# Kernel tuning notes

Hardware: AMD Instinct MI355X
Metric: run time of the kernel (lower is better)

## Reference

```python
import jax, jax.numpy as jnp
import numpy as np

IN_F, OUT_F, BLOCK, NBLK = 1024, 4096, 256, 16
TOPK = NBLK // 4  # 4, as in forward: n_blocks // 4


def setup_inputs() -> dict:
    key = jax.random.key(0)
    ks = jax.random.split(key, 7)
    s = 1.0 / np.sqrt(IN_F)
    s2 = 1.0 / np.sqrt(OUT_F)
    return {
        "x": jax.random.normal(ks[0], (4, 4096, IN_F), jnp.float32),
        "router_w": jax.random.uniform(ks[1], (NBLK, IN_F), jnp.float32, -s, s),
        "router_b": jax.random.uniform(ks[2], (NBLK,), jnp.float32, -s, s),
        "w1": jax.random.uniform(ks[3], (OUT_F, IN_F), jnp.float32, -s, s),
        "b1": jax.random.uniform(ks[4], (OUT_F,), jnp.float32, -s, s),
        "w2": jax.random.uniform(ks[5], (IN_F, OUT_F), jnp.float32, -s2, s2),
        "b2": jax.random.uniform(ks[6], (IN_F,), jnp.float32, -s2, s2),
    }


def reference(x, router_w, router_b, w1, b1, w2, b2):
    x_shape = x.shape
    xf = x.reshape(-1, IN_F)  # [N, d]
    n = xf.shape[0]
    # router: Linear + softmax, then top-k block selection per token
    prob = jax.nn.softmax(xf @ router_w.T + router_b, axis=-1)  # [N, n_blocks]
    _, idx = jax.lax.top_k(prob, TOPK)  # [N, k]
    mask = jnp.zeros((n, NBLK), bool).at[jnp.arange(n)[:, None], idx].set(True)
    # RoutedLinearRow: per-block fc1, zeros at unselected blocks
    w1b = w1.reshape(NBLK, BLOCK, IN_F)
    b1b = b1.reshape(NBLK, BLOCK)
    h = jnp.einsum('nd,ibd->nib', xf, w1b) + b1b  # [N, n_blocks, block]
    h = jnp.where(mask[:, :, None], h, jnp.zeros((), h.dtype))
    h = jax.nn.relu(h)
    # RoutedLinearCol: only selected blocks contribute
    w2b = w2.reshape(IN_F, NBLK, BLOCK)
    y = jnp.einsum('nib,dib->nd', jnp.where(mask[:, :, None], h, 0.0), w2b) + b2
    return y.reshape(x_shape)
```

## Files before the change

### kernel.cpp

```cpp
#include <hip/hip_runtime.h>
#include <hip/hip_bf16.h>

#define NTOK   16384
#define INF    1024
#define OUTF   4096
#define NBLK   16
#define BLKSZ  256
#define KTOP   4

typedef short bf16x8 __attribute__((ext_vector_type(8)));
typedef float f32x4 __attribute__((ext_vector_type(4)));
typedef unsigned short u16x8 __attribute__((ext_vector_type(8)));

__device__ __forceinline__ unsigned short f2bf(float f) {
  unsigned u = __float_as_uint(f);
  u += 0x7FFFu + ((u >> 16) & 1u);
  return (unsigned short)(u >> 16);
}

__device__ __forceinline__ void load_lds16(const void* g, void* l) {
  __builtin_amdgcn_global_load_lds(
      (const __attribute__((address_space(1))) unsigned int*)g,
      (__attribute__((address_space(3))) unsigned int*)l, 16, 0, 0);
}

__device__ __forceinline__ double shfl_xor_d(double v, int m) {
  long long l = __double_as_longlong(v);
  int lo = (int)(l & 0xFFFFFFFFll), hi = (int)(l >> 32);
  lo = __shfl_xor(lo, m);
  hi = __shfl_xor(hi, m);
  return __longlong_as_double(((long long)hi << 32) | (unsigned long long)(unsigned)lo);
}

__device__ __forceinline__ int pi_perm(int j) {
  return (j & 128) | ((j & 7) << 4) | ((j >> 3) & 15);
}

__global__ __launch_bounds__(256) void k_cvt_router(
    const float* __restrict__ x, const float* __restrict__ rw,
    const float* __restrict__ rb, const float* __restrict__ w1,
    const float* __restrict__ w2, const float* __restrict__ b1,
    unsigned* __restrict__ tok_blocks, unsigned* __restrict__ counts,
    unsigned short* __restrict__ xb, unsigned short* __restrict__ w1b,
    unsigned short* __restrict__ w2p, float* __restrict__ b1p) {
  __shared__ float4 rwl[4096];
  const int tid = threadIdx.x;
  const float4* rw4 = (const float4*)rw;
  for (int i = tid; i < 4096; i += 256) rwl[i] = rw4[i];
  __syncthreads();

  const int n = blockIdx.x * 32 + (tid >> 3);
  const int q = tid & 7;
  double p[16];
#pragma unroll
  for (int j = 0; j < 16; ++j) p[j] = 0.0;
  const float4* xr = (const float4*)(x + (size_t)n * INF);
  ushort4* xbr = (ushort4*)(xb + (size_t)n * INF);
#pragma unroll 4
  for (int i = 0; i < 32; ++i) {
    const int d4 = q + i * 8;
    const float4 xv = xr[d4];
    ushort4 o;
    o.x = f2bf(xv.x); o.y = f2bf(xv.y); o.z = f2bf(xv.z); o.w = f2bf(xv.w);
    xbr[d4] = o;
#pragma unroll
    for (int j = 0; j < 16; ++j) {
      const float4 wv = rwl[j * 256 + d4];
      p[j] = fma((double)xv.x, (double)wv.x, p[j]);
      p[j] = fma((double)xv.y, (double)wv.y, p[j]);
      p[j] = fma((double)xv.z, (double)wv.z, p[j]);
      p[j] = fma((double)xv.w, (double)wv.w, p[j]);
    }
  }
#pragma unroll
  for (int j = 0; j < 16; ++j) {
    double v = p[j];
    v += shfl_xor_d(v, 1);
    v += shfl_xor_d(v, 2);
    v += shfl_xor_d(v, 4);
    p[j] = v + (double)rb[j];
  }

  __syncthreads();
  unsigned* hist = (unsigned*)rwl;
  if (tid < 16) hist[tid] = 0;
  __syncthreads();

  if (q == 0) {
    unsigned packed = 0;
#pragma unroll
    for (int j = 0; j < 16; ++j) {
      int r = 0;
#pragma unroll
      for (int j2 = 0; j2 < 16; ++j2)
        r += (int)((p[j2] > p[j]) | ((p[j2] == p[j]) & (j2 < j)));
      if (r < KTOP) packed |= (unsigned)j << (8 * r);
    }
    tok_blocks[n] = packed;
    atomicAdd(&hist[packed & 15u], 1u);
    atomicAdd(&hist[(packed >> 8) & 15u], 1u);
    atomicAdd(&hist[(packed >> 16) & 15u], 1u);
    atomicAdd(&hist[(packed >> 24) & 15u], 1u);
  }
  __syncthreads();
  if (tid < 16 && hist[tid]) atomicAdd(&counts[tid], hist[tid]);

  const size_t stride = (size_t)gridDim.x * 256;
  for (size_t i = (size_t)blockIdx.x * 256 + tid; i < 1573376; i += stride) {
    if (i < 1048576) {
      float4 v = ((const float4*)w1)[i];
      ushort4 o;
      o.x = f2bf(v.x); o.y = f2bf(v.y); o.z = f2bf(v.z); o.w = f2bf(v.w);
      ((ushort4*)w1b)[i] = o;
    } else if (i < 1572864) {
      const size_t g = i - 1048576;
      const int d = (int)(g >> 9);
      const int rest = (int)(g & 511);
      const int jg = rest * 8;
      const int blk = jg >> 8;
      const int j0 = jg & 255;
      const float* src = w2 + (size_t)d * 4096 + blk * 256;
      u16x8 o;
#pragma unroll
      for (int ni = 0; ni < 8; ++ni) o[ni] = f2bf(src[pi_perm(j0 + ni)]);
      *(u16x8*)(w2p + (size_t)d * 4096 + jg) = o;
    } else {
      const int idx = (int)(i - 1572864);
      const int jg = idx * 8;
      const int blk = jg >> 8;
      const int j0 = jg & 255;
      const float* src = b1 + blk * 256;
      float o[8];
#pragma unroll
      for (int ni = 0; ni < 8; ++ni) o[ni] = src[pi_perm(j0 + ni)];
      float4* dst = (float4*)(b1p + jg);
      dst[0] = make_float4(o[0], o[1], o[2], o[3]);
      dst[1] = make_float4(o[4], o[5], o[6], o[7]);
    }
  }
}

__global__ __launch_bounds__(256) void k_build(
    const unsigned* __restrict__ tok_blocks, const unsigned* __restrict__ counts,
    unsigned* __restrict__ alloc, unsigned short* __restrict__ list) {
  unsigned offl[16];
  {
    unsigned o = 0;
#pragma unroll
    for (int i = 0; i < 16; ++i) { offl[i] = o; o += (counts[i] + 127u) & ~127u; }
  }
  const int n = blockIdx.x * 256 + threadIdx.x;
  const unsigned packed = tok_blocks[n];
  const int lane = threadIdx.x & 63;
#pragma unroll
  for (int b = 0; b < 16; ++b) {
    int r = -1;
#pragma unroll
    for (int q = 0; q < 4; ++q)
      if (((packed >> (8 * q)) & 15u) == (unsigned)b) r = q;
    unsigned long long m = __ballot(r >= 0);
    if (m) {
      int leader = __ffsll((unsigned long long)m) - 1;
      unsigned base = 0;
      if (lane == leader) base = offl[b] + atomicAdd(&alloc[b], (unsigned)__popcll(m));
      base = (unsigned)__shfl((int)base, leader);
      if (r >= 0) {
        unsigned pos = base + (unsigned)__popcll(m & ((1ull << lane) - 1ull));
        list[pos] = (unsigned short)(n | (r << 14));
      }
    }
  }
}

__global__ __launch_bounds__(256, 1) void k_ffn(
    const unsigned short* __restrict__ xb, const unsigned short* __restrict__ w1b,
    const unsigned short* __restrict__ w2p, const float* __restrict__ b1p,
    const unsigned short* __restrict__ list, const unsigned* __restrict__ counts,
    unsigned short* __restrict__ part) {
  __shared__ __align__(16) char lds[163840];
  char* const As0 = lds + 65536;
  char* const As1 = lds + 81920;
  char* const Bs0 = lds + 98304;
  char* const Bs1 = lds + 131072;

  const int bid0 = blockIdx.x;
  const int bid = (bid0 & 7) * 256 + (bid0 >> 3);
  const int blk = bid >> 7;
  const int tile = bid & 127;
  unsigned cnt = 0, goffBase = 0;
  {
    unsigned o = 0;
#pragma unroll
    for (int i = 0; i < 16; ++i) {
      const unsigned c = counts[i];
      if (i == blk) { cnt = c; goffBase = o; }
      o += (c + 127u) & ~127u;
    }
  }
  if ((unsigned)(tile * 128) >= cnt) return;
  const unsigned goff = goffBase + tile * 128;
  const int rem = (int)cnt - tile * 128;

  const int tid = threadIdx.x;
  const int lane = tid & 63;
  const int wid = tid >> 6;
  const int wr = wid >> 1;
  const int wc = wid & 1;
  const int c16 = lane & 15;
  const int aChunk = (tid & 7) ^ ((tid >> 3) & 7);

  unsigned tok[4];
#pragma unroll
  for (int l = 0; l < 4; ++l) tok[l] = list[goff + (tid >> 3) + l * 32] & 0x3FFFu;

#define STAGE_A(buf, k0)                                                        \
  _Pragma("unroll")                                                             \
  for (int l = 0; l < 4; ++l)                                                   \
    load_lds16(xb + (size_t)tok[l] * 1024 + (k0) + aChunk * 8,                  \
               (buf) + (l * 256 + wid * 64) * 16);

#define STAGE_B1(buf, k0)                                                       \
  _Pragma("unroll")                                                             \
  for (int l = 0; l < 8; ++l)                                                   \
    load_lds16(w1b + (size_t)(blk * 256 + l * 32 + (tid >> 3)) * 1024 + (k0) +  \
                   aChunk * 8,                                                  \
               (buf) + (l * 256 + wid * 64) * 16);

#define COMPUTE_A(abuf, bbuf)                                                   \
  _Pragma("unroll")                                                             \
  for (int ks = 0; ks < 2; ++ks) {                                              \
    const int kc = ks * 4 + (lane >> 4);                                        \
    bf16x8 a[4], b[8];                                                          \
    _Pragma("unroll")                                                           \
    for (int mi = 0; mi < 4; ++mi) {                                            \
      const int row = wr * 64 + mi * 16 + c16;                                  \
      a[mi] = *(const bf16x8*)((abuf) + row * 128 + ((kc ^ (row & 7)) << 4));   \
    }                                                                           \
    _Pragma("unroll")                                                           \
    for (int ni = 0; ni < 8; ++ni) {                                            \
      const int row = wc * 128 + ni * 16 + c16;                                 \
      b[ni] = *(const bf16x8*)((bbuf) + row * 128 + ((kc ^ (row & 7)) << 4));   \
    }                                                                           \
    _Pragma("unroll")                                                           \
    for (int mi = 0; mi < 4; ++mi)                                              \
      _Pragma("unroll")                                                         \
      for (int ni = 0; ni < 8; ++ni)                                            \
        acc[mi][ni] =                                                           \
            __builtin_amdgcn_mfma_f32_16x16x32_bf16(a[mi], b[ni], acc[mi][ni], 0, 0, 0); \
  }

  f32x4 acc[4][8] = {};
  STAGE_A(As0, 0);
  STAGE_B1(Bs0, 0);
  __syncthreads();
#pragma unroll 1
  for (int kk = 0; kk < 8; ++kk) {
    const int k0 = kk * 128;
    STAGE_A(As1, k0 + 64);
    STAGE_B1(Bs1, k0 + 64);
    COMPUTE_A(As0, Bs0);
    __syncthreads();
    if (kk < 7) {
      STAGE_A(As0, k0 + 128);
      STAGE_B1(Bs0, k0 + 128);
    }
    COMPUTE_A(As1, Bs1);
    __syncthreads();
  }

#define STAGE_B2(buf, it)                                                       \
  {                                                                             \
    const int ns2 = (it) >> 2, k02 = ((it) & 3) * 64;                           \
    _Pragma("unroll")                                                           \
    for (int l = 0; l < 8; ++l)                                                 \
      load_lds16(w2p + (size_t)(ns2 * 256 + l * 32 + (tid >> 3)) * 4096 +       \
                     blk * 256 + k02 + aChunk * 8,                              \
                 (buf) + (l * 256 + wid * 64) * 16);                            \
  }

#define COMPUTE_B(bbuf, k02)                                                    \
  _Pragma("unroll")                                                             \
  for (int ks = 0; ks < 2; ++ks) {                                              \
    const int kc = ks * 4 + (lane >> 4);                                        \
    bf16x8 a[4], b[8];                                                          \
    _Pragma("unroll")                                                           \
    for (int mi = 0; mi < 4; ++mi) {                                            \
      const int row = wr * 64 + mi * 16 + c16;                                  \
      a[mi] = *(const bf16x8*)(lds + row * 512 + (k02) * 2 +                    \
                               ((kc ^ (row & 7)) << 4));                        \
    }                                                                           \
    _Pragma("unroll")                                                           \
    for (int ni = 0; ni < 8; ++ni) {                                            \
      const int row = wc * 128 + ni * 16 + c16;                                 \
      b[ni] = *(const bf16x8*)((bbuf) + row * 128 + ((kc ^ (row & 7)) << 4));   \
    }                                                                           \
    _Pragma("unroll")                                                           \
    for (int mi = 0; mi < 4; ++mi)                                              \
      _Pragma("unroll")                                                         \
      for (int ni = 0; ni < 8; ++ni)                                            \
        acc2[mi][ni] =                                                          \
            __builtin_amdgcn_mfma_f32_16x16x32_bf16(a[mi], b[ni], acc2[mi][ni], 0, 0, 0); \
  }

  STAGE_B2(Bs0, 0);

  {
    const float4* bp = (const float4*)(b1p + blk * 256 + wc * 128 + c16 * 8);
    const float4 bv0 = bp[0], bv1 = bp[1];
    const float bvv[8] = {bv0.x, bv0.y, bv0.z, bv0.w, bv1.x, bv1.y, bv1.z, bv1.w};
    const int chunk = wc * 16 + c16;
    const int cslot = (chunk & ~7);
    const int clow  = (chunk & 7);
#pragma unroll
    for (int mi = 0; mi < 4; ++mi) {
#pragma unroll
      for (int i = 0; i < 4; ++i) {
        const int row = wr * 64 + mi * 16 + (lane >> 4) * 4 + i;
        u16x8 wv;
#pragma unroll
        for (int ni = 0; ni < 8; ++ni) {
          float v = acc[mi][ni][i] + bvv[ni];
          v = v > 0.f ? v : 0.f;
          wv[ni] = f2bf(v);
        }
        *(u16x8*)(lds + row * 512 + ((cslot | (clow ^ (row & 7))) << 4)) = wv;
      }
    }
  }
  __syncthreads();

#pragma unroll 1
  for (int ns = 0; ns < 4; ++ns) {
    f32x4 acc2[4][8] = {};
    const int it0 = ns * 4;
    STAGE_B2(Bs1, it0 + 1);
    COMPUTE_B(Bs0, 0);
    __syncthreads();
    STAGE_B2(Bs0, it0 + 2);
    COMPUTE_B(Bs1, 64);
    __syncthreads();
    STAGE_B2(Bs1, it0 + 3);
    COMPUTE_B(Bs0, 128);
    __syncthreads();
    if (ns < 3) STAGE_B2(Bs0, it0 + 4);
    COMPUTE_B(Bs1, 192);
    __syncthreads();
#pragma unroll
    for (int mi = 0; mi < 4; ++mi) {
#pragma unroll
      for (int i = 0; i < 4; ++i) {
        const int row = wr * 64 + mi * 16 + (lane >> 4) * 4 + i;
        if (row < rem) {
          const unsigned e = list[goff + row];
          u16x8 wv;
#pragma unroll
          for (int ni = 0; ni < 8; ++ni) wv[ni] = f2bf(acc2[mi][ni][i]);
          *(u16x8*)(part + ((size_t)(e & 0x3FFFu) * 4 + (e >> 14)) * 1024 +
                    ns * 256 + wc * 128 + c16 * 8) = wv;
        }
      }
    }
  }
#undef STAGE_A
#undef STAGE_B1
#undef STAGE_B2
#undef COMPUTE_A
#undef COMPUTE_B
}

__global__ __launch_bounds__(256) void k_reduce(const unsigned short* __restrict__ part,
                                                const float* __restrict__ b2,
                                                float* __restrict__ out) {
  __shared__ float lds[8 * 1028];
  const int tid = threadIdx.x;
  const int tok0 = blockIdx.x * 8;
  const int tok_l = tid >> 5;
  const int l32 = tid & 31;
  const unsigned short* pbase = part + (size_t)(tok0 + tok_l) * 4096;

#pragma unroll
  for (int g = 0; g < 4; ++g) {
    const int idx = g * 32 + l32;
    const int p0 = idx * 8;
    float s[8] = {0.f, 0.f, 0.f, 0.f, 0.f, 0.f, 0.f, 0.f};
#pragma unroll
    for (int sl = 0; sl < 4; ++sl) {
      u16x8 v = *(const u16x8*)(pbase + sl * 1024 + p0);
#pragma unroll
      for (int j = 0; j < 8; ++j)
        s[j] += __uint_as_float((unsigned)(unsigned short)v[j] << 16);
    }
    const int ns = idx >> 5, wcb = (idx >> 4) & 1, cc = idx & 15;
#pragma unroll
    for (int ni = 0; ni < 8; ++ni)
      lds[tok_l * 1028 + ns * 256 + wcb * 128 + ni * 16 + cc] = s[ni];
  }
  __syncthreads();
  const float4 b2v = ((const float4*)b2)[tid];
#pragma unroll
  for (int r = 0; r < 8; ++r) {
    f32x4 lv = *(f32x4*)&lds[r * 1028 + tid * 4];
    float4 o = make_float4(lv[0] + b2v.x, lv[1] + b2v.y, lv[2] + b2v.z, lv[3] + b2v.w);
    *(float4*)(out + (size_t)(tok0 + r) * 1024 + tid * 4) = o;
  }
}

extern "C" void kernel_launch(void* const* d_in, const int* in_sizes, int n_in,
                              void* d_out, int out_size, void* d_ws, size_t ws_size,
                              hipStream_t stream) {
  const float* x  = (const float*)d_in[0];
  const float* rw = (const float*)d_in[1];
  const float* rb = (const float*)d_in[2];
  const float* w1 = (const float*)d_in[3];
  const float* b1 = (const float*)d_in[4];
  const float* w2 = (const float*)d_in[5];
  const float* b2 = (const float*)d_in[6];
  float* out = (float*)d_out;

  char* ws = (char*)d_ws;
  unsigned short* part = (unsigned short*)(ws);
  unsigned short* xb   = (unsigned short*)(ws + 134217728);
  unsigned short* w1b  = (unsigned short*)(ws + 167772160);
  unsigned short* w2p  = (unsigned short*)(ws + 176160768);
  unsigned* tokb       = (unsigned*)(ws + 184549376);
  unsigned short* list = (unsigned short*)(ws + 184614912);
  float* b1p           = (float*)(ws + 184750080);
  unsigned* counts     = (unsigned*)(ws + 184766464);
  unsigned* alloc      = (unsigned*)(ws + 184766528);

  hipMemsetAsync(ws + 184766464, 0, 128, stream);
  k_cvt_router<<<dim3(512), dim3(256), 0, stream>>>(x, rw, rb, w1, w2, b1, tokb,
                                                    counts, xb, w1b, w2p, b1p);
  k_build<<<dim3(64), dim3(256), 0, stream>>>(tokb, counts, alloc, list);
  k_ffn<<<dim3(2048), dim3(256), 0, stream>>>(xb, w1b, w2p, b1p, list, counts, part);
  k_reduce<<<dim3(2048), dim3(256), 0, stream>>>(part, b2, out);
}
```

Before: 290.6 us.

## Split FFN workgroup across 8 waves with 64x64 per-wave tiles

```diff
diff --git a/kernel.cpp b/kernel.cpp
--- a/kernel.cpp
+++ b/kernel.cpp
@@ -11,6 +11,7 @@
 typedef short bf16x8 __attribute__((ext_vector_type(8)));
 typedef float f32x4 __attribute__((ext_vector_type(4)));
 typedef unsigned short u16x8 __attribute__((ext_vector_type(8)));
+typedef unsigned short u16x4 __attribute__((ext_vector_type(4)));
 
 __device__ __forceinline__ unsigned short f2bf(float f) {
   unsigned u = __float_as_uint(f);
@@ -32,8 +33,8 @@
   return __longlong_as_double(((long long)hi << 32) | (unsigned long long)(unsigned)lo);
 }
 
-__device__ __forceinline__ int pi_perm(int j) {
-  return (j & 128) | ((j & 7) << 4) | ((j >> 3) & 15);
+__device__ __forceinline__ int pi2(int j) {
+  return (j & 192) | ((j & 3) << 4) | ((j >> 2) & 15);
 }
 
 __global__ __launch_bounds__(256) void k_cvt_router(
@@ -122,7 +123,7 @@
       const float* src = w2 + (size_t)d * 4096 + blk * 256;
       u16x8 o;
 #pragma unroll
-      for (int ni = 0; ni < 8; ++ni) o[ni] = f2bf(src[pi_perm(j0 + ni)]);
+      for (int ni = 0; ni < 8; ++ni) o[ni] = f2bf(src[pi2(j0 + ni)]);
       *(u16x8*)(w2p + (size_t)d * 4096 + jg) = o;
     } else {
       const int idx = (int)(i - 1572864);
@@ -132,7 +133,7 @@
       const float* src = b1 + blk * 256;
       float o[8];
 #pragma unroll
-      for (int ni = 0; ni < 8; ++ni) o[ni] = src[pi_perm(j0 + ni)];
+      for (int ni = 0; ni < 8; ++ni) o[ni] = src[pi2(j0 + ni)];
       float4* dst = (float4*)(b1p + jg);
       dst[0] = make_float4(o[0], o[1], o[2], o[3]);
       dst[1] = make_float4(o[4], o[5], o[6], o[7]);
@@ -172,7 +173,7 @@
   }
 }
 
-__global__ __launch_bounds__(256, 1) void k_ffn(
+__global__ __launch_bounds__(512, 1) void k_ffn(
     const unsigned short* __restrict__ xb, const unsigned short* __restrict__ w1b,
     const unsigned short* __restrict__ w2p, const float* __restrict__ b1p,
     const unsigned short* __restrict__ list, const unsigned* __restrict__ counts,
@@ -204,52 +205,57 @@
   const int tid = threadIdx.x;
   const int lane = tid & 63;
   const int wid = tid >> 6;
-  const int wr = wid >> 1;
-  const int wc = wid & 1;
+  const int wr = wid >> 2;
+  const int wc = wid & 3;
+  const int asl = tid & 7;
   const int c16 = lane & 15;
-  const int aChunk = (tid & 7) ^ ((tid >> 3) & 7);
-
-  unsigned tok[4];
-#pragma unroll
-  for (int l = 0; l < 4; ++l) tok[l] = list[goff + (tid >> 3) + l * 32] & 0x3FFFu;
+
+  const unsigned tok0 = list[goff + (tid >> 3)] & 0x3FFFu;
+  const unsigned tok1 = list[goff + 64 + (tid >> 3)] & 0x3FFFu;
+  const int arow0 = tid >> 3;
+  const int arow1 = 64 + arow0;
 
 #define STAGE_A(buf, k0)                                                        \
-  _Pragma("unroll")                                                             \
-  for (int l = 0; l < 4; ++l)                                                   \
-    load_lds16(xb + (size_t)tok[l] * 1024 + (k0) + aChunk * 8,                  \
-               (buf) + (l * 256 + wid * 64) * 16);
+  {                                                                             \
+    load_lds16(xb + (size_t)tok0 * INF + (k0) + (asl ^ (arow0 & 7)) * 8,        \
+               (buf) + (wid * 64) * 16);                                        \
+    load_lds16(xb + (size_t)tok1 * INF + (k0) + (asl ^ (arow1 & 7)) * 8,        \
+               (buf) + (512 + wid * 64) * 16);                                  \
+  }
 
 #define STAGE_B1(buf, k0)                                                       \
   _Pragma("unroll")                                                             \
-  for (int l = 0; l < 8; ++l)                                                   \
-    load_lds16(w1b + (size_t)(blk * 256 + l * 32 + (tid >> 3)) * 1024 + (k0) +  \
-                   aChunk * 8,                                                  \
-               (buf) + (l * 256 + wid * 64) * 16);
+  for (int r = 0; r < 4; ++r) {                                                 \
+    const int row = (r * 512 + tid) >> 3;                                       \
+    load_lds16(w1b + ((size_t)(blk * 256 + row)) * INF + (k0) +                 \
+                   (asl ^ (row & 7)) * 8,                                       \
+               (buf) + (r * 512 + wid * 64) * 16);                              \
+  }
 
 #define COMPUTE_A(abuf, bbuf)                                                   \
   _Pragma("unroll")                                                             \
   for (int ks = 0; ks < 2; ++ks) {                                              \
     const int kc = ks * 4 + (lane >> 4);                                        \
-    bf16x8 a[4], b[8];                                                          \
+    bf16x8 a[4], b[4];                                                          \
     _Pragma("unroll")                                                           \
     for (int mi = 0; mi < 4; ++mi) {                                            \
       const int row = wr * 64 + mi * 16 + c16;                                  \
       a[mi] = *(const bf16x8*)((abuf) + row * 128 + ((kc ^ (row & 7)) << 4));   \
     }                                                                           \
     _Pragma("unroll")                                                           \
-    for (int ni = 0; ni < 8; ++ni) {                                            \
-      const int row = wc * 128 + ni * 16 + c16;                                 \
+    for (int ni = 0; ni < 4; ++ni) {                                            \
+      const int row = wc * 64 + ni * 16 + c16;                                  \
       b[ni] = *(const bf16x8*)((bbuf) + row * 128 + ((kc ^ (row & 7)) << 4));   \
     }                                                                           \
     _Pragma("unroll")                                                           \
     for (int mi = 0; mi < 4; ++mi)                                              \
       _Pragma("unroll")                                                         \
-      for (int ni = 0; ni < 8; ++ni)                                            \
+      for (int ni = 0; ni < 4; ++ni)                                            \
         acc[mi][ni] =                                                           \
             __builtin_amdgcn_mfma_f32_16x16x32_bf16(a[mi], b[ni], acc[mi][ni], 0, 0, 0); \
   }
 
-  f32x4 acc[4][8] = {};
+  f32x4 acc[4][4] = {};
   STAGE_A(As0, 0);
   STAGE_B1(Bs0, 0);
   __syncthreads();
@@ -272,17 +278,19 @@
   {                                                                             \
     const int ns2 = (it) >> 2, k02 = ((it) & 3) * 64;                           \
     _Pragma("unroll")                                                           \
-    for (int l = 0; l < 8; ++l)                                                 \
-      load_lds16(w2p + (size_t)(ns2 * 256 + l * 32 + (tid >> 3)) * 4096 +       \
-                     blk * 256 + k02 + aChunk * 8,                              \
-                 (buf) + (l * 256 + wid * 64) * 16);                            \
+    for (int r = 0; r < 4; ++r) {                                               \
+      const int row = (r * 512 + tid) >> 3;                                     \
+      load_lds16(w2p + (size_t)(ns2 * 256 + row) * OUTF + blk * 256 + k02 +     \
+                     (asl ^ (row & 7)) * 8,                                     \
+                 (buf) + (r * 512 + wid * 64) * 16);                            \
+    }                                                                           \
   }
 
 #define COMPUTE_B(bbuf, k02)                                                    \
   _Pragma("unroll")                                                             \
   for (int ks = 0; ks < 2; ++ks) {                                              \
     const int kc = ks * 4 + (lane >> 4);                                        \
-    bf16x8 a[4], b[8];                                                          \
+    bf16x8 a[4], b[4];                                                          \
     _Pragma("unroll")                                                           \
     for (int mi = 0; mi < 4; ++mi) {                                            \
       const int row = wr * 64 + mi * 16 + c16;                                  \
@@ -290,14 +298,14 @@
                                ((kc ^ (row & 7)) << 4));                        \
     }                                                                           \
     _Pragma("unroll")                                                           \
-    for (int ni = 0; ni < 8; ++ni) {                                            \
-      const int row = wc * 128 + ni * 16 + c16;                                 \
+    for (int ni = 0; ni < 4; ++ni) {                                            \
+      const int row = wc * 64 + ni * 16 + c16;                                  \
       b[ni] = *(const bf16x8*)((bbuf) + row * 128 + ((kc ^ (row & 7)) << 4));   \
     }                                                                           \
     _Pragma("unroll")                                                           \
     for (int mi = 0; mi < 4; ++mi)                                              \
       _Pragma("unroll")                                                         \
-      for (int ni = 0; ni < 8; ++ni)                                            \
+      for (int ni = 0; ni < 4; ++ni)                                            \
         acc2[mi][ni] =                                                          \
             __builtin_amdgcn_mfma_f32_16x16x32_bf16(a[mi], b[ni], acc2[mi][ni], 0, 0, 0); \
   }
@@ -305,25 +313,22 @@
   STAGE_B2(Bs0, 0);
 
   {
-    const float4* bp = (const float4*)(b1p + blk * 256 + wc * 128 + c16 * 8);
-    const float4 bv0 = bp[0], bv1 = bp[1];
-    const float bvv[8] = {bv0.x, bv0.y, bv0.z, bv0.w, bv1.x, bv1.y, bv1.z, bv1.w};
-    const int chunk = wc * 16 + c16;
-    const int cslot = (chunk & ~7);
-    const int clow  = (chunk & 7);
+    const float4 bv = *(const float4*)(b1p + blk * 256 + wc * 64 + c16 * 4);
+    const float bvv[4] = {bv.x, bv.y, bv.z, bv.w};
 #pragma unroll
     for (int mi = 0; mi < 4; ++mi) {
 #pragma unroll
       for (int i = 0; i < 4; ++i) {
         const int row = wr * 64 + mi * 16 + (lane >> 4) * 4 + i;
-        u16x8 wv;
-#pragma unroll
-        for (int ni = 0; ni < 8; ++ni) {
+        u16x4 wv;
+#pragma unroll
+        for (int ni = 0; ni < 4; ++ni) {
           float v = acc[mi][ni][i] + bvv[ni];
           v = v > 0.f ? v : 0.f;
           wv[ni] = f2bf(v);
         }
-        *(u16x8*)(lds + row * 512 + ((cslot | (clow ^ (row & 7))) << 4)) = wv;
+        *(u16x4*)(lds + row * 512 +
+                  ((wc * 8 + (((c16 >> 1)) ^ (row & 7))) << 4) + (c16 & 1) * 8) = wv;
       }
     }
   }
@@ -331,7 +336,7 @@
 
 #pragma unroll 1
   for (int ns = 0; ns < 4; ++ns) {
-    f32x4 acc2[4][8] = {};
+    f32x4 acc2[4][4] = {};
     const int it0 = ns * 4;
     STAGE_B2(Bs1, it0 + 1);
     COMPUTE_B(Bs0, 0);
@@ -352,11 +357,11 @@
         const int row = wr * 64 + mi * 16 + (lane >> 4) * 4 + i;
         if (row < rem) {
           const unsigned e = list[goff + row];
-          u16x8 wv;
-#pragma unroll
-          for (int ni = 0; ni < 8; ++ni) wv[ni] = f2bf(acc2[mi][ni][i]);
-          *(u16x8*)(part + ((size_t)(e & 0x3FFFu) * 4 + (e >> 14)) * 1024 +
-                    ns * 256 + wc * 128 + c16 * 8) = wv;
+          u16x4 wv;
+#pragma unroll
+          for (int ni = 0; ni < 4; ++ni) wv[ni] = f2bf(acc2[mi][ni][i]);
+          *(u16x4*)(part + ((size_t)(e & 0x3FFFu) * 4 + (e >> 14)) * 1024 +
+                    ns * 256 + wc * 64 + c16 * 4) = wv;
         }
       }
     }
@@ -379,8 +384,8 @@
   const unsigned short* pbase = part + (size_t)(tok0 + tok_l) * 4096;
 
 #pragma unroll
-  for (int g = 0; g < 4; ++g) {
-    const int idx = g * 32 + l32;
+  for (int g4 = 0; g4 < 4; ++g4) {
+    const int idx = g4 * 32 + l32;
     const int p0 = idx * 8;
     float s[8] = {0.f, 0.f, 0.f, 0.f, 0.f, 0.f, 0.f, 0.f};
 #pragma unroll
@@ -390,10 +395,13 @@
       for (int j = 0; j < 8; ++j)
         s[j] += __uint_as_float((unsigned)(unsigned short)v[j] << 16);
     }
-    const int ns = idx >> 5, wcb = (idx >> 4) & 1, cc = idx & 15;
-#pragma unroll
-    for (int ni = 0; ni < 8; ++ni)
-      lds[tok_l * 1028 + ns * 256 + wcb * 128 + ni * 16 + cc] = s[ni];
+    const int g = idx >> 5, r = idx & 31;
+    const int wcb = r >> 3, c16b = (r & 7) * 2;
+#pragma unroll
+    for (int j = 0; j < 8; ++j) {
+      const int ni = j & 3, cc = c16b + (j >> 2);
+      lds[tok_l * 1028 + g * 256 + wcb * 64 + ni * 16 + cc] = s[j];
+    }
   }
   __syncthreads();
   const float4 b2v = ((const float4*)b2)[tid];
@@ -432,6 +440,6 @@
   k_cvt_router<<<dim3(512), dim3(256), 0, stream>>>(x, rw, rb, w1, w2, b1, tokb,
                                                     counts, xb, w1b, w2p, b1p);
   k_build<<<dim3(64), dim3(256), 0, stream>>>(tokb, counts, alloc, list);
-  k_ffn<<<dim3(2048), dim3(256), 0, stream>>>(xb, w1b, w2p, b1p, list, counts, part);
+  k_ffn<<<dim3(2048), dim3(512), 0, stream>>>(xb, w1b, w2p, b1p, list, counts, part);
   k_reduce<<<dim3(2048), dim3(256), 0, stream>>>(part, b2, out);
 }
```

Result: faster. 274.7 us (-5.5%).

## Halve FFN token tile and K step to fit two blocks per CU

Applied to the files above, without the earlier changes.

```diff
diff --git a/kernel.cpp b/kernel.cpp
--- a/kernel.cpp
+++ b/kernel.cpp
@@ -172,16 +172,16 @@
   }
 }
 
-__global__ __launch_bounds__(256, 1) void k_ffn(
+__global__ __launch_bounds__(256, 2) void k_ffn(
     const unsigned short* __restrict__ xb, const unsigned short* __restrict__ w1b,
     const unsigned short* __restrict__ w2p, const float* __restrict__ b1p,
     const unsigned short* __restrict__ list, const unsigned* __restrict__ counts,
     unsigned short* __restrict__ part) {
-  __shared__ __align__(16) char lds[163840];
-  char* const As0 = lds + 65536;
-  char* const As1 = lds + 81920;
-  char* const Bs0 = lds + 98304;
-  char* const Bs1 = lds + 131072;
+  __shared__ __align__(16) char lds[73728];
+  char* const As0 = lds + 32768;
+  char* const As1 = lds + 36864;
+  char* const Bs0 = lds + 40960;
+  char* const Bs1 = lds + 57344;
 
   const int bid0 = blockIdx.x;
   const int bid = (bid0 & 7) * 256 + (bid0 >> 3);
@@ -197,9 +197,9 @@
       o += (c + 127u) & ~127u;
     }
   }
-  if ((unsigned)(tile * 128) >= cnt) return;
-  const unsigned goff = goffBase + tile * 128;
-  const int rem = (int)cnt - tile * 128;
+  if ((unsigned)(tile * 64) >= cnt) return;
+  const unsigned goff = goffBase + tile * 64;
+  const int rem = (int)cnt - tile * 64;
 
   const int tid = threadIdx.x;
   const int lane = tid & 63;
@@ -207,62 +207,64 @@
   const int wr = wid >> 1;
   const int wc = wid & 1;
   const int c16 = lane & 15;
-  const int aChunk = (tid & 7) ^ ((tid >> 3) & 7);
-
-  unsigned tok[4];
-#pragma unroll
-  for (int l = 0; l < 4; ++l) tok[l] = list[goff + (tid >> 3) + l * 32] & 0x3FFFu;
+  const int kc = lane >> 4;
+
+  const int srow = tid >> 2;
+  const int schunk = tid & 3;
+  const unsigned tokS = list[goff + srow] & 0x3FFFu;
 
 #define STAGE_A(buf, k0)                                                        \
-  _Pragma("unroll")                                                             \
-  for (int l = 0; l < 4; ++l)                                                   \
-    load_lds16(xb + (size_t)tok[l] * 1024 + (k0) + aChunk * 8,                  \
-               (buf) + (l * 256 + wid * 64) * 16);
+  load_lds16(xb + (size_t)tokS * INF + (k0) +                                   \
+                 ((schunk ^ ((srow >> 1) & 3)) * 8),                            \
+             (buf) + tid * 16);
 
 #define STAGE_B1(buf, k0)                                                       \
   _Pragma("unroll")                                                             \
-  for (int l = 0; l < 8; ++l)                                                   \
-    load_lds16(w1b + (size_t)(blk * 256 + l * 32 + (tid >> 3)) * 1024 + (k0) +  \
-                   aChunk * 8,                                                  \
-               (buf) + (l * 256 + wid * 64) * 16);
+  for (int l = 0; l < 4; ++l) {                                                 \
+    const int idx = l * 256 + tid;                                              \
+    const int row = idx >> 2;                                                   \
+    load_lds16(w1b + (size_t)(blk * 256 + row) * INF + (k0) +                   \
+                   (((idx & 3) ^ ((row >> 1) & 3)) * 8),                        \
+               (buf) + idx * 16);                                               \
+  }
 
 #define COMPUTE_A(abuf, bbuf)                                                   \
-  _Pragma("unroll")                                                             \
-  for (int ks = 0; ks < 2; ++ks) {                                              \
-    const int kc = ks * 4 + (lane >> 4);                                        \
-    bf16x8 a[4], b[8];                                                          \
-    _Pragma("unroll")                                                           \
-    for (int mi = 0; mi < 4; ++mi) {                                            \
-      const int row = wr * 64 + mi * 16 + c16;                                  \
-      a[mi] = *(const bf16x8*)((abuf) + row * 128 + ((kc ^ (row & 7)) << 4));   \
+  {                                                                             \
+    bf16x8 a[2], b[8];                                                          \
+    _Pragma("unroll")                                                           \
+    for (int mi = 0; mi < 2; ++mi) {                                            \
+      const int row = wr * 32 + mi * 16 + c16;                                  \
+      a[mi] = *(const bf16x8*)((abuf) + row * 64 +                              \
+                               ((kc ^ ((row >> 1) & 3)) << 4));                 \
     }                                                                           \
     _Pragma("unroll")                                                           \
     for (int ni = 0; ni < 8; ++ni) {                                            \
       const int row = wc * 128 + ni * 16 + c16;                                 \
-      b[ni] = *(const bf16x8*)((bbuf) + row * 128 + ((kc ^ (row & 7)) << 4));   \
+      b[ni] = *(const bf16x8*)((bbuf) + row * 64 +                              \
+                               ((kc ^ ((row >> 1) & 3)) << 4));                 \
     }                                                                           \
     _Pragma("unroll")                                                           \
-    for (int mi = 0; mi < 4; ++mi)                                              \
+    for (int mi = 0; mi < 2; ++mi)                                              \
       _Pragma("unroll")                                                         \
       for (int ni = 0; ni < 8; ++ni)                                            \
         acc[mi][ni] =                                                           \
             __builtin_amdgcn_mfma_f32_16x16x32_bf16(a[mi], b[ni], acc[mi][ni], 0, 0, 0); \
   }
 
-  f32x4 acc[4][8] = {};
+  f32x4 acc[2][8] = {};
   STAGE_A(As0, 0);
   STAGE_B1(Bs0, 0);
   __syncthreads();
 #pragma unroll 1
-  for (int kk = 0; kk < 8; ++kk) {
-    const int k0 = kk * 128;
-    STAGE_A(As1, k0 + 64);
-    STAGE_B1(Bs1, k0 + 64);
+  for (int kk = 0; kk < 16; ++kk) {
+    const int k0 = kk * 64;
+    STAGE_A(As1, k0 + 32);
+    STAGE_B1(Bs1, k0 + 32);
     COMPUTE_A(As0, Bs0);
     __syncthreads();
-    if (kk < 7) {
-      STAGE_A(As0, k0 + 128);
-      STAGE_B1(Bs0, k0 + 128);
+    if (kk < 15) {
+      STAGE_A(As0, k0 + 64);
+      STAGE_B1(Bs0, k0 + 64);
     }
     COMPUTE_A(As1, Bs1);
     __syncthreads();
@@ -270,32 +272,35 @@
 
 #define STAGE_B2(buf, it)                                                       \
   {                                                                             \
-    const int ns2 = (it) >> 2, k02 = ((it) & 3) * 64;                           \
-    _Pragma("unroll")                                                           \
-    for (int l = 0; l < 8; ++l)                                                 \
-      load_lds16(w2p + (size_t)(ns2 * 256 + l * 32 + (tid >> 3)) * 4096 +       \
-                     blk * 256 + k02 + aChunk * 8,                              \
-                 (buf) + (l * 256 + wid * 64) * 16);                            \
+    const int ns2 = (it) >> 3, k02 = ((it) & 7) * 32;                           \
+    _Pragma("unroll")                                                           \
+    for (int l = 0; l < 4; ++l) {                                               \
+      const int idx = l * 256 + tid;                                            \
+      const int row = idx >> 2;                                                 \
+      load_lds16(w2p + (size_t)(ns2 * 256 + row) * OUTF + blk * 256 + k02 +     \
+                     (((idx & 3) ^ ((row >> 1) & 3)) * 8),                      \
+                 (buf) + idx * 16);                                             \
+    }                                                                           \
   }
 
 #define COMPUTE_B(bbuf, k02)                                                    \
-  _Pragma("unroll")                                                             \
-  for (int ks = 0; ks < 2; ++ks) {                                              \
-    const int kc = ks * 4 + (lane >> 4);                                        \
-    bf16x8 a[4], b[8];                                                          \
-    _Pragma("unroll")                                                           \
-    for (int mi = 0; mi < 4; ++mi) {                                            \
-      const int row = wr * 64 + mi * 16 + c16;                                  \
-      a[mi] = *(const bf16x8*)(lds + row * 512 + (k02) * 2 +                    \
-                               ((kc ^ (row & 7)) << 4));                        \
+  {                                                                             \
+    bf16x8 a[2], b[8];                                                          \
+    _Pragma("unroll")                                                           \
+    for (int mi = 0; mi < 2; ++mi) {                                            \
+      const int row = wr * 32 + mi * 16 + c16;                                  \
+      const int co = ((k02) >> 3) + kc;                                         \
+      a[mi] = *(const bf16x8*)(lds + row * 512 +                                \
+                               (((co & ~7) | ((co & 7) ^ (row & 7))) << 4));    \
     }                                                                           \
     _Pragma("unroll")                                                           \
     for (int ni = 0; ni < 8; ++ni) {                                            \
       const int row = wc * 128 + ni * 16 + c16;                                 \
-      b[ni] = *(const bf16x8*)((bbuf) + row * 128 + ((kc ^ (row & 7)) << 4));   \
+      b[ni] = *(const bf16x8*)((bbuf) + row * 64 +                              \
+                               ((kc ^ ((row >> 1) & 3)) << 4));                 \
     }                                                                           \
     _Pragma("unroll")                                                           \
-    for (int mi = 0; mi < 4; ++mi)                                              \
+    for (int mi = 0; mi < 2; ++mi)                                              \
       _Pragma("unroll")                                                         \
       for (int ni = 0; ni < 8; ++ni)                                            \
         acc2[mi][ni] =                                                          \
@@ -312,10 +317,10 @@
     const int cslot = (chunk & ~7);
     const int clow  = (chunk & 7);
 #pragma unroll
-    for (int mi = 0; mi < 4; ++mi) {
+    for (int mi = 0; mi < 2; ++mi) {
 #pragma unroll
       for (int i = 0; i < 4; ++i) {
-        const int row = wr * 64 + mi * 16 + (lane >> 4) * 4 + i;
+        const int row = wr * 32 + mi * 16 + (lane >> 4) * 4 + i;
         u16x8 wv;
 #pragma unroll
         for (int ni = 0; ni < 8; ++ni) {
@@ -331,25 +336,22 @@
 
 #pragma unroll 1
   for (int ns = 0; ns < 4; ++ns) {
-    f32x4 acc2[4][8] = {};
-    const int it0 = ns * 4;
-    STAGE_B2(Bs1, it0 + 1);
-    COMPUTE_B(Bs0, 0);
-    __syncthreads();
-    STAGE_B2(Bs0, it0 + 2);
-    COMPUTE_B(Bs1, 64);
-    __syncthreads();
-    STAGE_B2(Bs1, it0 + 3);
-    COMPUTE_B(Bs0, 128);
-    __syncthreads();
-    if (ns < 3) STAGE_B2(Bs0, it0 + 4);
-    COMPUTE_B(Bs1, 192);
-    __syncthreads();
-#pragma unroll
-    for (int mi = 0; mi < 4; ++mi) {
+    f32x4 acc2[2][8] = {};
+#pragma unroll 1
+    for (int jj = 0; jj < 4; ++jj) {
+      const int it = ns * 8 + jj * 2;
+      STAGE_B2(Bs1, it + 1);
+      COMPUTE_B(Bs0, jj * 64);
+      __syncthreads();
+      if (it + 2 < 32) STAGE_B2(Bs0, it + 2);
+      COMPUTE_B(Bs1, jj * 64 + 32);
+      __syncthreads();
+    }
+#pragma unroll
+    for (int mi = 0; mi < 2; ++mi) {
 #pragma unroll
       for (int i = 0; i < 4; ++i) {
-        const int row = wr * 64 + mi * 16 + (lane >> 4) * 4 + i;
+        const int row = wr * 32 + mi * 16 + (lane >> 4) * 4 + i;
         if (row < rem) {
           const unsigned e = list[goff + row];
           u16x8 wv;
```

Measured after the change: 287.1 us. No clear change (-1.2%).
